# Optimization experiments

Hardware: AMD Instinct MI355X
Metric: run time of the kernel (lower is better)

The kernel has to match this reference:

```python
import jax, jax.numpy as jnp
import numpy as np

B, N, IN_DIM, HEADS, PER_HEAD = 8, 512, 256, 4, 32
OUT_DIM = HEADS * PER_HEAD  # 128
NEG_SLOPE = 0.2


def setup_inputs() -> dict:
    key = jax.random.key(0)
    ks = jax.random.split(key, 8)
    x = jax.random.normal(ks[0], (B, N, IN_DIM), jnp.float32)
    adj = jax.random.randint(ks[1], (B, N, N), 0, 2, jnp.int32)
    sl = 1.0 / np.sqrt(IN_DIM)
    W_l = jax.random.normal(ks[2], (IN_DIM, OUT_DIM), jnp.float32) * sl  # source proj
    b_l = jnp.zeros((OUT_DIM,), jnp.float32)
    W_r = jax.random.normal(ks[3], (IN_DIM, OUT_DIM), jnp.float32) * sl  # target proj
    b_r = jnp.zeros((OUT_DIM,), jnp.float32)
    att = jax.random.normal(ks[4], (HEADS, PER_HEAD), jnp.float32) * (1.0 / np.sqrt(PER_HEAD))
    bias = jnp.zeros((OUT_DIM,), jnp.float32)
    return {"x": x, "adj": adj, "W_l": W_l, "b_l": b_l, "W_r": W_r, "b_r": b_r,
            "att": att, "bias": bias}


def _gatv2_single(x_b, adj_b, W_l, b_l, W_r, b_r, att, bias):
    # PyG GATv2Conv: remove_self_loops + add_self_loops -> diagonal forced to 1
    n = x_b.shape[0]
    adj_sl = jnp.fill_diagonal(adj_b, 1, inplace=False)
    # edge_index = adj.nonzero().t(): source = row, target = col
    m = (adj_sl != 0).T  # m[i, j]: source j feeds target i
    xl = (x_b @ W_l + b_l).reshape(n, HEADS, PER_HEAD)  # source-side features
    xr = (x_b @ W_r + b_r).reshape(n, HEADS, PER_HEAD)  # target-side features
    s = xr[:, None] + xl[None, :]                       # [i, j, H, C]
    s = jnp.where(s > 0, s, NEG_SLOPE * s)              # LeakyReLU(0.2)
    e = jnp.einsum('ijhc,hc->ijh', s, att)              # attention logits
    e = jnp.where(m[..., None], e, -jnp.inf)
    alpha = jax.nn.softmax(e, axis=1)                   # softmax over sources j
    out = jnp.einsum('ijh,jhc->ihc', alpha, xl).reshape(n, HEADS * PER_HEAD)
    return out + bias


def reference(x, adj, W_l, b_l, W_r, b_r, att, bias):
    # Sequential per-batch processing, faithful to the original Python loop
    # and keeping the [N,N,H,C] intermediate to one graph at a time.
    def one(args):
        x_b, adj_b = args
        return _gatv2_single(x_b, adj_b, W_l, b_l, W_r, b_r, att, bias)
    return jax.lax.map(one, (x, adj))  # [B, N, OUT_DIM]
```

## Files before the change

kernel.cpp:

```cpp
#include <hip/hip_runtime.h>
#include <hip/hip_bf16.h>

#define B_   8
#define N_   512
#define IND  256
#define H_   4
#define PH   32
#define OD   128
#define TI   4

typedef float v2f __attribute__((ext_vector_type(2)));

#define ATT_SCALE 0.5770780163555854f
#define DLR_SCALE 0.8656170245333781f

template <int PAT>
__device__ __forceinline__ float dpp_add(float x) {
    int yi = __builtin_amdgcn_mov_dpp(__float_as_int(x), PAT, 0xF, 0xF, true);
    return x + __int_as_float(yi);
}

__device__ __forceinline__ float fast_exp2(float x) {
#if __has_builtin(__builtin_amdgcn_exp2f)
    return __builtin_amdgcn_exp2f(x);
#else
    return exp2f(x);
#endif
}

__device__ __forceinline__ void pk_fma(v2f& d, v2f a, v2f b) {
    asm("v_pk_fma_f32 %0, %1, %2, %0" : "+v"(d) : "v"(a), "v"(b));
}

__global__ __launch_bounds__(256, 2) void proj_kernel(
    const float* __restrict__ x,
    const float* __restrict__ Wl, const float* __restrict__ bl,
    const float* __restrict__ Wr, const float* __restrict__ br,
    const float* __restrict__ att,
    float* __restrict__ xl, float* __restrict__ xr,
    float* __restrict__ dl, float* __restrict__ dr)
{
    __shared__ float xs[8 * IND];
    const int t = threadIdx.x;
    const int row0 = blockIdx.x * 8;

    const float4* xp4 = (const float4*)(x + (size_t)row0 * IND);
    float4* xs4 = (float4*)xs;
    #pragma unroll
    for (int k = 0; k < 2; ++k)
        xs4[t + k * 256] = xp4[t + k * 256];
    __syncthreads();

    const int which = t >> 7;
    const int rg = (t >> 6) & 1;
    const int og = t & 63;
    const int o0 = og * 2;
    const int r0 = rg * 4;
    const float* W  = which ? Wr : Wl;
    const float* bb = which ? br : bl;

    float acc0[4], acc1[4];
    #pragma unroll
    for (int r = 0; r < 4; ++r) { acc0[r] = 0.f; acc1[r] = 0.f; }

    for (int k = 0; k < IND; k += 4) {
        float wf0[4], wf1[4];
        #pragma unroll
        for (int kk = 0; kk < 4; ++kk) {
            float2 wv = *(const float2*)(W + (size_t)(k + kk) * OD + o0);
            wf0[kk] = wv.x;
            wf1[kk] = wv.y;
        }
        float xv[4][4];
        #pragma unroll
        for (int r = 0; r < 4; ++r)
            *(float4*)(xv[r]) = *(const float4*)(&xs[(r0 + r) * IND + k]);
        #pragma unroll
        for (int kk = 0; kk < 4; ++kk)
            #pragma unroll
            for (int r = 0; r < 4; ++r) {
                acc0[r] = fmaf(xv[r][kk], wf0[kk], acc0[r]);
                acc1[r] = fmaf(xv[r][kk], wf1[kk], acc1[r]);
            }
    }

    const float bv0 = bb[o0];
    const float bv1 = bb[o0 + 1];
    const float a0 = att[o0];
    const float a1 = att[o0 + 1];
    float* dst = which ? xr : xl;
    float* dp  = which ? dr : dl;
    float dcon[4];
    #pragma unroll
    for (int r = 0; r < 4; ++r) {
        float y0 = acc0[r] + bv0;
        float y1 = acc1[r] + bv1;
        *(float2*)(&dst[(size_t)(row0 + r0 + r) * OD + o0]) = make_float2(y0, y1);
        dcon[r] = fmaf(a0, y0, a1 * y1);
    }
    #pragma unroll
    for (int m = 1; m < 16; m <<= 1) {
        #pragma unroll
        for (int r = 0; r < 4; ++r)
            dcon[r] += __shfl_xor(dcon[r], m);
    }
    if ((og & 15) == 0) {
        const int h = og >> 4;
        #pragma unroll
        for (int r = 0; r < 4; ++r)
            dp[(size_t)(row0 + r0 + r) * H_ + h] = DLR_SCALE * dcon[r];
    }
}

__global__ __launch_bounds__(256, 3) void attn_kernel(
    const int* __restrict__ adj, const float* __restrict__ att,
    const float* __restrict__ bias,
    const float* __restrict__ xl, const float* __restrict__ xr,
    const float* __restrict__ dl, const float* __restrict__ dr,
    float* __restrict__ out)
{
    __shared__ float sacc[H_][16][TI][PH];
    __shared__ float ssum[H_][16][TI];

    const int t = threadIdx.x;
    const int b  = blockIdx.x >> 7;
    const int i0 = (blockIdx.x & 127) * TI;
    const int cq = t & 3;
    const int js = (t >> 2) & 15;
    const int h  = t >> 6;
    const int cbase = h * PH + cq * 8;

    float atS[8];
    {
        const float* ap = att + cbase;
        float4 a0 = *(const float4*)(ap);
        float4 a1 = *(const float4*)(ap + 4);
        atS[0] = ATT_SCALE * a0.x; atS[1] = ATT_SCALE * a0.y;
        atS[2] = ATT_SCALE * a0.z; atS[3] = ATT_SCALE * a0.w;
        atS[4] = ATT_SCALE * a1.x; atS[5] = ATT_SCALE * a1.y;
        atS[6] = ATT_SCALE * a1.z; atS[7] = ATT_SCALE * a1.w;
    }
    float xrS[TI][8];
    float drv[TI];
    #pragma unroll
    for (int il = 0; il < TI; ++il) {
        const float* xp = xr + ((size_t)(b * N_ + i0 + il)) * OD + cbase;
        float4 r0 = *(const float4*)(xp);
        float4 r1 = *(const float4*)(xp + 4);
        xrS[il][0] = r0.x; xrS[il][1] = r0.y; xrS[il][2] = r0.z; xrS[il][3] = r0.w;
        xrS[il][4] = r1.x; xrS[il][5] = r1.y; xrS[il][6] = r1.z; xrS[il][7] = r1.w;
        drv[il] = dr[((size_t)(b * N_ + i0 + il)) * H_ + h];
    }

    v2f acc[TI][4];
    float sumw[TI];
    #pragma unroll
    for (int il = 0; il < TI; ++il) {
        sumw[il] = 0.f;
        #pragma unroll
        for (int m = 0; m < 4; ++m) acc[il][m] = (v2f){0.f, 0.f};
    }

    const float* xlp = xl + ((size_t)(b * N_ + js)) * OD + cbase;
    const int*   ajp = adj + ((size_t)(b * N_ + js)) * N_ + i0;
    const float* dlp = dl + ((size_t)(b * N_ + js)) * H_ + h;

    float4 va = *(const float4*)(xlp);
    float4 vb = *(const float4*)(xlp + 4);
    int4   mj = *(const int4*)(ajp);
    float  dj = *dlp;

    #pragma unroll 2
    for (int u = 0; u < 32; ++u) {
        float4 wa = va, wb = vb;
        int4   wm = mj;
        float  wd = dj;
        if (u < 31) {
            xlp += 16 * OD; ajp += 16 * N_; dlp += 16 * H_;
            va = *(const float4*)(xlp);
            vb = *(const float4*)(xlp + 4);
            mj = *(const int4*)(ajp);
            dj = *dlp;
        }
        const int j = u * 16 + js;
        v2f p0 = (v2f){wa.x, wa.y}, p1 = (v2f){wa.z, wa.w};
        v2f p2 = (v2f){wb.x, wb.y}, p3 = (v2f){wb.z, wb.w};
        int wmv[4] = {wm.x, wm.y, wm.z, wm.w};
        #pragma unroll
        for (int il = 0; il < TI; ++il) {
            float s, e2a = 0.f, e2b = 0.f;
            s = xrS[il][0] + wa.x; e2a = fmaf(atS[0], __builtin_fabsf(s), e2a);
            s = xrS[il][1] + wa.y; e2b = fmaf(atS[1], __builtin_fabsf(s), e2b);
            s = xrS[il][2] + wa.z; e2a = fmaf(atS[2], __builtin_fabsf(s), e2a);
            s = xrS[il][3] + wa.w; e2b = fmaf(atS[3], __builtin_fabsf(s), e2b);
            s = xrS[il][4] + wb.x; e2a = fmaf(atS[4], __builtin_fabsf(s), e2a);
            s = xrS[il][5] + wb.y; e2b = fmaf(atS[5], __builtin_fabsf(s), e2b);
            s = xrS[il][6] + wb.z; e2a = fmaf(atS[6], __builtin_fabsf(s), e2a);
            s = xrS[il][7] + wb.w; e2b = fmaf(atS[7], __builtin_fabsf(s), e2b);
            float eh = e2a + e2b;
            eh = dpp_add<0xB1>(eh);
            eh = dpp_add<0x4E>(eh);
            float e = (wd + drv[il]) + eh;
            bool keep = (wmv[il] != 0) || (j == i0 + il);
            float w = keep ? fast_exp2(e) : 0.f;
            sumw[il] += w;
            v2f ws = (v2f){w, w};
            pk_fma(acc[il][0], ws, p0);
            pk_fma(acc[il][1], ws, p1);
            pk_fma(acc[il][2], ws, p2);
            pk_fma(acc[il][3], ws, p3);
        }
    }

    #pragma unroll
    for (int il = 0; il < TI; ++il) {
        float4 w0 = make_float4(acc[il][0].x, acc[il][0].y,
                                acc[il][1].x, acc[il][1].y);
        float4 w1 = make_float4(acc[il][2].x, acc[il][2].y,
                                acc[il][3].x, acc[il][3].y);
        *(float4*)(&sacc[h][js][il][cq * 8])     = w0;
        *(float4*)(&sacc[h][js][il][cq * 8 + 4]) = w1;
    }
    if (cq == 0) {
        #pragma unroll
        for (int il = 0; il < TI; ++il)
            ssum[h][js][il] = sumw[il];
    }
    __syncthreads();

    const int lane = t & 63;
    const int o = lane * 2;
    const int il2 = o >> 5;
    const int c2 = o & 31;
    float st = 0.f;
    #pragma unroll
    for (int k = 0; k < 16; ++k) st += ssum[h][k][il2];
    float a0 = 0.f, a1 = 0.f;
    #pragma unroll
    for (int k = 0; k < 16; ++k) {
        float2 p = *(const float2*)(&sacc[h][k][il2][c2]);
        a0 += p.x; a1 += p.y;
    }
    const float inv = 1.f / st;
    const int c = h * PH + c2;
    float* op = out + ((size_t)(b * N_ + i0 + il2)) * OD;
    *(float2*)(&op[c]) = make_float2(fmaf(a0, inv, bias[c]),
                                     fmaf(a1, inv, bias[c + 1]));
}

extern "C" void kernel_launch(void* const* d_in, const int* in_sizes, int n_in,
                              void* d_out, int out_size, void* d_ws, size_t ws_size,
                              hipStream_t stream) {
    const float* x    = (const float*)d_in[0];
    const int*   adj  = (const int*)d_in[1];
    const float* Wl   = (const float*)d_in[2];
    const float* bl   = (const float*)d_in[3];
    const float* Wr   = (const float*)d_in[4];
    const float* br   = (const float*)d_in[5];
    const float* att  = (const float*)d_in[6];
    const float* bias = (const float*)d_in[7];
    float* out = (float*)d_out;

    float* xl = (float*)d_ws;
    float* xr = xl + (size_t)B_ * N_ * OD;
    float* dl = xr + (size_t)B_ * N_ * OD;
    float* dr = dl + (size_t)B_ * N_ * H_;

    proj_kernel<<<512, 256, 0, stream>>>(x, Wl, bl, Wr, br, att, xl, xr, dl, dr);
    attn_kernel<<<1024, 256, 0, stream>>>(adj, att, bias, xl, xr, dl, dr, out);
}
```

Measured before the change: 122.0 us.

## Halve attention target tile, restructure projection tiling, remap blocks across batches

```diff
diff --git a/kernel.cpp b/kernel.cpp
--- a/kernel.cpp
+++ b/kernel.cpp
@@ -1,5 +1,4 @@
 #include <hip/hip_runtime.h>
-#include <hip/hip_bf16.h>
 
 #define B_   8
 #define N_   512
@@ -7,7 +6,7 @@
 #define H_   4
 #define PH   32
 #define OD   128
-#define TI   4
+#define TI   2
 
 typedef float v2f __attribute__((ext_vector_type(2)));
 
@@ -32,7 +31,7 @@
     asm("v_pk_fma_f32 %0, %1, %2, %0" : "+v"(d) : "v"(a), "v"(b));
 }
 
-__global__ __launch_bounds__(256, 2) void proj_kernel(
+__global__ __launch_bounds__(256, 4) void proj_kernel(
     const float* __restrict__ x,
     const float* __restrict__ Wl, const float* __restrict__ bl,
     const float* __restrict__ Wr, const float* __restrict__ br,
@@ -40,91 +39,78 @@
     float* __restrict__ xl, float* __restrict__ xr,
     float* __restrict__ dl, float* __restrict__ dr)
 {
-    __shared__ float xs[8 * IND];
     const int t = threadIdx.x;
-    const int row0 = blockIdx.x * 8;
-
-    const float4* xp4 = (const float4*)(x + (size_t)row0 * IND);
-    float4* xs4 = (float4*)xs;
-    #pragma unroll
-    for (int k = 0; k < 2; ++k)
-        xs4[t + k * 256] = xp4[t + k * 256];
-    __syncthreads();
-
+    const int row0 = blockIdx.x * 4;
+
+    const int r     = t & 3;
+    const int og    = (t >> 2) & 31;
     const int which = t >> 7;
-    const int rg = (t >> 6) & 1;
-    const int og = t & 63;
-    const int o0 = og * 2;
-    const int r0 = rg * 4;
-    const float* W  = which ? Wr : Wl;
+    const int o0 = og * 4;
+    const float* W = (which ? Wr : Wl) + o0;
+    const float* xrow = x + (size_t)(row0 + r) * IND;
+
+    float acc[4] = {0.f, 0.f, 0.f, 0.f};
+
+    float4 wb[2][4];
+    float4 xb[2];
+    #pragma unroll
+    for (int kk = 0; kk < 4; ++kk)
+        wb[0][kk] = *(const float4*)(W + (size_t)kk * OD);
+    xb[0] = *(const float4*)(xrow);
+
+    #pragma unroll 2
+    for (int s = 0; s < 64; ++s) {
+        const int cur = s & 1, nxt = cur ^ 1;
+        if (s < 63) {
+            const float* Wq = W + (size_t)((s + 1) * 4) * OD;
+            #pragma unroll
+            for (int kk = 0; kk < 4; ++kk)
+                wb[nxt][kk] = *(const float4*)(Wq + (size_t)kk * OD);
+            xb[nxt] = *(const float4*)(xrow + (s + 1) * 4);
+        }
+        const float xk[4] = {xb[cur].x, xb[cur].y, xb[cur].z, xb[cur].w};
+        #pragma unroll
+        for (int kk = 0; kk < 4; ++kk) {
+            acc[0] = fmaf(xk[kk], wb[cur][kk].x, acc[0]);
+            acc[1] = fmaf(xk[kk], wb[cur][kk].y, acc[1]);
+            acc[2] = fmaf(xk[kk], wb[cur][kk].z, acc[2]);
+            acc[3] = fmaf(xk[kk], wb[cur][kk].w, acc[3]);
+        }
+    }
+
     const float* bb = which ? br : bl;
-
-    float acc0[4], acc1[4];
-    #pragma unroll
-    for (int r = 0; r < 4; ++r) { acc0[r] = 0.f; acc1[r] = 0.f; }
-
-    for (int k = 0; k < IND; k += 4) {
-        float wf0[4], wf1[4];
-        #pragma unroll
-        for (int kk = 0; kk < 4; ++kk) {
-            float2 wv = *(const float2*)(W + (size_t)(k + kk) * OD + o0);
-            wf0[kk] = wv.x;
-            wf1[kk] = wv.y;
-        }
-        float xv[4][4];
-        #pragma unroll
-        for (int r = 0; r < 4; ++r)
-            *(float4*)(xv[r]) = *(const float4*)(&xs[(r0 + r) * IND + k]);
-        #pragma unroll
-        for (int kk = 0; kk < 4; ++kk)
-            #pragma unroll
-            for (int r = 0; r < 4; ++r) {
-                acc0[r] = fmaf(xv[r][kk], wf0[kk], acc0[r]);
-                acc1[r] = fmaf(xv[r][kk], wf1[kk], acc1[r]);
-            }
-    }
-
-    const float bv0 = bb[o0];
-    const float bv1 = bb[o0 + 1];
-    const float a0 = att[o0];
-    const float a1 = att[o0 + 1];
     float* dst = which ? xr : xl;
     float* dp  = which ? dr : dl;
-    float dcon[4];
-    #pragma unroll
-    for (int r = 0; r < 4; ++r) {
-        float y0 = acc0[r] + bv0;
-        float y1 = acc1[r] + bv1;
-        *(float2*)(&dst[(size_t)(row0 + r0 + r) * OD + o0]) = make_float2(y0, y1);
-        dcon[r] = fmaf(a0, y0, a1 * y1);
-    }
-    #pragma unroll
-    for (int m = 1; m < 16; m <<= 1) {
-        #pragma unroll
-        for (int r = 0; r < 4; ++r)
-            dcon[r] += __shfl_xor(dcon[r], m);
-    }
-    if ((og & 15) == 0) {
-        const int h = og >> 4;
-        #pragma unroll
-        for (int r = 0; r < 4; ++r)
-            dp[(size_t)(row0 + r0 + r) * H_ + h] = DLR_SCALE * dcon[r];
-    }
-}
-
-__global__ __launch_bounds__(256, 3) void attn_kernel(
+    float4 bv = *(const float4*)(bb + o0);
+    float4 av = *(const float4*)(att + o0);
+    const float y0 = acc[0] + bv.x;
+    const float y1 = acc[1] + bv.y;
+    const float y2 = acc[2] + bv.z;
+    const float y3 = acc[3] + bv.w;
+    *(float4*)(&dst[(size_t)(row0 + r) * OD + o0]) = make_float4(y0, y1, y2, y3);
+
+    float dc = fmaf(av.x, y0, fmaf(av.y, y1, fmaf(av.z, y2, av.w * y3)));
+    dc += __shfl_xor(dc, 4);
+    dc += __shfl_xor(dc, 8);
+    dc += __shfl_xor(dc, 16);
+    if (((t >> 2) & 7) == 0)
+        dp[(size_t)(row0 + r) * H_ + (og >> 3)] = DLR_SCALE * dc;
+}
+
+__global__ __launch_bounds__(256, 6) void attn_kernel(
     const int* __restrict__ adj, const float* __restrict__ att,
     const float* __restrict__ bias,
     const float* __restrict__ xl, const float* __restrict__ xr,
     const float* __restrict__ dl, const float* __restrict__ dr,
     float* __restrict__ out)
 {
-    __shared__ float sacc[H_][16][TI][PH];
+    __shared__ float sacc[H_][TI][16][PH + 1];
     __shared__ float ssum[H_][16][TI];
 
     const int t = threadIdx.x;
-    const int b  = blockIdx.x >> 7;
-    const int i0 = (blockIdx.x & 127) * TI;
+    const int bid = (blockIdx.x & 7) * 256 + (blockIdx.x >> 3);
+    const int b  = bid >> 8;
+    const int i0 = (bid & 255) * TI;
     const int cq = t & 3;
     const int js = (t >> 2) & 15;
     const int h  = t >> 6;
@@ -167,25 +153,25 @@
 
     float4 va = *(const float4*)(xlp);
     float4 vb = *(const float4*)(xlp + 4);
-    int4   mj = *(const int4*)(ajp);
+    int2   mj = *(const int2*)(ajp);
     float  dj = *dlp;
 
     #pragma unroll 2
     for (int u = 0; u < 32; ++u) {
         float4 wa = va, wb = vb;
-        int4   wm = mj;
+        int2   wm = mj;
         float  wd = dj;
         if (u < 31) {
             xlp += 16 * OD; ajp += 16 * N_; dlp += 16 * H_;
             va = *(const float4*)(xlp);
             vb = *(const float4*)(xlp + 4);
-            mj = *(const int4*)(ajp);
+            mj = *(const int2*)(ajp);
             dj = *dlp;
         }
         const int j = u * 16 + js;
         v2f p0 = (v2f){wa.x, wa.y}, p1 = (v2f){wa.z, wa.w};
         v2f p2 = (v2f){wb.x, wb.y}, p3 = (v2f){wb.z, wb.w};
-        int wmv[4] = {wm.x, wm.y, wm.z, wm.w};
+        int wmv[TI] = {wm.x, wm.y};
         #pragma unroll
         for (int il = 0; il < TI; ++il) {
             float s, e2a = 0.f, e2b = 0.f;
@@ -218,8 +204,8 @@
                                 acc[il][1].x, acc[il][1].y);
         float4 w1 = make_float4(acc[il][2].x, acc[il][2].y,
                                 acc[il][3].x, acc[il][3].y);
-        *(float4*)(&sacc[h][js][il][cq * 8])     = w0;
-        *(float4*)(&sacc[h][js][il][cq * 8 + 4]) = w1;
+        *(float4*)(&sacc[h][il][js][cq * 8])     = w0;
+        *(float4*)(&sacc[h][il][js][cq * 8 + 4]) = w1;
     }
     if (cq == 0) {
         #pragma unroll
@@ -229,23 +215,17 @@
     __syncthreads();
 
     const int lane = t & 63;
-    const int o = lane * 2;
-    const int il2 = o >> 5;
-    const int c2 = o & 31;
+    const int il2  = lane >> 5;
+    const int c    = lane & 31;
     float st = 0.f;
     #pragma unroll
     for (int k = 0; k < 16; ++k) st += ssum[h][k][il2];
-    float a0 = 0.f, a1 = 0.f;
-    #pragma unroll
-    for (int k = 0; k < 16; ++k) {
-        float2 p = *(const float2*)(&sacc[h][k][il2][c2]);
-        a0 += p.x; a1 += p.y;
-    }
+    float a = 0.f;
+    #pragma unroll
+    for (int k = 0; k < 16; ++k) a += sacc[h][il2][k][c];
     const float inv = 1.f / st;
-    const int c = h * PH + c2;
-    float* op = out + ((size_t)(b * N_ + i0 + il2)) * OD;
-    *(float2*)(&op[c]) = make_float2(fmaf(a0, inv, bias[c]),
-                                     fmaf(a1, inv, bias[c + 1]));
+    const int cg = h * PH + c;
+    out[((size_t)(b * N_ + i0 + il2)) * OD + cg] = fmaf(a, inv, bias[cg]);
 }
 
 extern "C" void kernel_launch(void* const* d_in, const int* in_sizes, int n_in,
@@ -266,6 +246,6 @@
     float* dl = xr + (size_t)B_ * N_ * OD;
     float* dr = dl + (size_t)B_ * N_ * H_;
 
-    proj_kernel<<<512, 256, 0, stream>>>(x, Wl, bl, Wr, br, att, xl, xr, dl, dr);
-    attn_kernel<<<1024, 256, 0, stream>>>(adj, att, bias, xl, xr, dl, dr, out);
-}
+    proj_kernel<<<1024, 256, 0, stream>>>(x, Wl, bl, Wr, br, att, xl, xr, dl, dr);
+    attn_kernel<<<2048, 256, 0, stream>>>(adj, att, bias, xl, xr, dl, dr, out);
+}
```

New measurement: 210.2 us. 72.4% more time.
